# Optimization experiments

Measured on AMD Instinct MI355X. Metric: run time of the kernel, lower is better.

Reference implementation:

```python
import jax, jax.numpy as jnp
import numpy as np

# Static configuration (matches init_kwargs / input_specs)
B = 4          # number of point clouds (equal-sized)
NPER = 4096    # points per cloud
RATIO = 0.25
MPER = int(NPER * RATIO)  # sampled centroids per cloud
R = 0.2        # ball-query radius
K = 64         # max_num_neighbors
C = 64         # feature dim


def setup_inputs() -> dict:
    key = jax.random.key(0)
    ks = jax.random.split(key, 6)
    N = B * NPER
    x = jax.random.normal(ks[0], (N, C), dtype=jnp.float32)
    pos = jax.random.uniform(ks[1], (N, 3), dtype=jnp.float32)
    batch = (jnp.arange(N) // NPER).astype(jnp.int64)
    weight = jax.random.normal(ks[2], (N,), dtype=jnp.float32)
    # local_nn = Seq(Lin(67,128), ReLU, Lin(128,256), ReLU)
    W1 = jax.random.normal(ks[3], (C + 3, 128), dtype=jnp.float32) / np.float32(np.sqrt(C + 3))
    b1 = jnp.zeros((128,), dtype=jnp.float32)
    W2 = jax.random.normal(ks[4], (128, 256), dtype=jnp.float32) / np.float32(np.sqrt(128))
    b2 = jnp.zeros((256,), dtype=jnp.float32)
    return {"x": x, "pos": pos, "batch": batch, "weight": weight,
            "W1": W1, "b1": b1, "W2": W2, "b2": b2}


def _fps_single(p):
    """Farthest point sampling on one cloud p:[NPER,3] -> MPER int32 indices.
    Deterministic start at index 0 (torch_geometric uses a random start)."""
    n = p.shape[0]
    def step(carry, _):
        mind, last = carry
        d = jnp.sum((p - p[last]) ** 2, axis=-1)
        mind = jnp.minimum(mind, d)
        nxt = jnp.argmax(mind).astype(jnp.int32)
        return (mind, nxt), last
    init = (jnp.full((n,), jnp.inf, dtype=p.dtype), jnp.int32(0))
    _, idx = jax.lax.scan(step, init, None, length=MPER)
    return idx  # [MPER]


def reference(x, pos, batch, weight, W1, b1, W2, b2):
    pos_b = pos.reshape(B, NPER, 3)
    x_b = x.reshape(B, NPER, C)

    # --- FPS per cloud (vectorized over clouds) ---
    idx = jax.vmap(_fps_single)(pos_b)                      # [B, MPER] local indices

    qpos = jnp.take_along_axis(pos_b, idx[:, :, None], axis=1)  # [B, MPER, 3]

    # --- radius ball query: K nearest within r (fixed-size, batch-respecting) ---
    d2 = jnp.sum((qpos[:, :, None, :] - pos_b[:, None, :, :]) ** 2, axis=-1)  # [B,MPER,NPER]
    neg, nbr = jax.lax.top_k(-d2, K)                        # [B, MPER, K]
    valid = (-neg) <= jnp.float32(R * R)                    # [B, MPER, K]

    # --- gather neighbor features / positions ---
    flat = nbr.reshape(B, MPER * K)
    x_j = jnp.take_along_axis(x_b, flat[:, :, None], axis=1).reshape(B, MPER, K, C)
    pos_j = jnp.take_along_axis(pos_b, flat[:, :, None], axis=1).reshape(B, MPER, K, 3)
    rel = pos_j - qpos[:, :, None, :]                       # [B, MPER, K, 3]

    # --- PointNetConv: local_nn(concat(x_j, rel)) then max aggregation ---
    msg = jnp.concatenate([x_j, rel], axis=-1)              # [B, MPER, K, C+3]
    h = jax.nn.relu(jnp.einsum('bmkc,cd->bmkd', msg, W1) + b1)
    h = jax.nn.relu(jnp.einsum('bmkd,de->bmke', h, W2) + b2)
    h = jnp.where(valid[:, :, :, None], h, -jnp.inf)
    x_out = jnp.max(h, axis=2).reshape(B * MPER, -1)        # [B*MPER, 256]

    # --- gather sampled pos / batch / weight using global indices ---
    idx_g = (idx + (jnp.arange(B, dtype=jnp.int32) * NPER)[:, None]).reshape(-1)
    pos_out = pos[idx_g]
    batch_out = batch[idx_g]
    weight_out = weight[idx_g]
    return x_out, pos_out, batch_out, weight_out
```

## Files before the change

kernel.cpp:

```cpp
#include <hip/hip_runtime.h>

#define NPER 4096
#define MPER 1024
#define KNB 64
#define NB 4
#define CAP 1024

typedef __attribute__((ext_vector_type(8))) short short8_t;
typedef __attribute__((ext_vector_type(4))) float f32x4;
typedef __attribute__((ext_vector_type(2))) float f32x2;

__device__ __forceinline__ unsigned short f2bf(float f) {
  union { float f; unsigned u; } v; v.f = f;
  unsigned r = v.u + 0x7fffu + ((v.u >> 16) & 1u);
  return (unsigned short)(r >> 16);
}

__device__ __forceinline__ f32x2 pk_add(f32x2 a, f32x2 b) {
  f32x2 d; asm("v_pk_add_f32 %0, %1, %2" : "=v"(d) : "v"(a), "v"(b)); return d;
}
__device__ __forceinline__ f32x2 pk_mul(f32x2 a, f32x2 b) {
  f32x2 d; asm("v_pk_mul_f32 %0, %1, %2" : "=v"(d) : "v"(a), "v"(b)); return d;
}

__device__ __forceinline__ void lds_barrier() {
  asm volatile("s_waitcnt lgkmcnt(0)" ::: "memory");
  __builtin_amdgcn_s_barrier();
  asm volatile("" ::: "memory");
}

#define DPP_KEY_STEP(ctrl)                                                            \
  {                                                                                   \
    unsigned lo = (unsigned)k, hi = (unsigned)(k >> 32);                              \
    unsigned tlo = (unsigned)__builtin_amdgcn_update_dpp((int)lo, (int)lo, ctrl, 0xF, 0xF, false); \
    unsigned thi = (unsigned)__builtin_amdgcn_update_dpp((int)hi, (int)hi, ctrl, 0xF, 0xF, false); \
    unsigned long long tk = ((unsigned long long)thi << 32) | tlo;                    \
    if (tk > k) k = tk;                                                               \
  }

#define U64MAX(a, b) (((a) > (b)) ? (a) : (b))

__global__ __launch_bounds__(256) void prep_kernel(const float* __restrict__ W1,
                                                   const float* __restrict__ W2,
                                                   unsigned short* __restrict__ w1f,
                                                   unsigned short* __restrict__ w2f,
                                                   int* __restrict__ idxg,
                                                   int* __restrict__ control) {
  const int f = blockIdx.x * 256 + threadIdx.x;
  if (f < 12288) {
    const int frag = f >> 9, r = f & 511, lane = r >> 3, e = r & 7;
    const int nt = frag / 3, kt = frag % 3;
    const int n = nt * 16 + (lane & 15);
    const int k = kt * 32 + (lane >> 4) * 8 + e;
    float v = (k < 67) ? W1[k * 128 + n] : 0.f;
    w1f[f] = f2bf(v);
  } else if (f < 45056) {
    const int g = f - 12288;
    const int frag = g >> 9, r = g & 511, lane = r >> 3, e = r & 7;
    const int nt = frag >> 2, kt = frag & 3;
    const int n = nt * 16 + (lane & 15);
    const int k = kt * 32 + (lane >> 4) * 8 + e;
    w2f[g] = f2bf(W2[k * 256 + n]);
  } else if (f < 45056 + NB * MPER) {
    idxg[f - 45056] = -1;
  } else if (f < 45056 + NB * MPER + 8) {
    control[f - 45056 - NB * MPER] = 0;
  }
}

__global__ __launch_bounds__(256) void fused_kernel(const float* __restrict__ x,
                                                    const float* __restrict__ pos,
                                                    const float* __restrict__ weight,
                                                    const unsigned short* __restrict__ w1f,
                                                    const unsigned short* __restrict__ w2f,
                                                    const float* __restrict__ b1,
                                                    const float* __restrict__ b2,
                                                    int* __restrict__ idxg,
                                                    int* __restrict__ control,
                                                    float* __restrict__ out) {
  __shared__ float4 p4[NPER];
  __shared__ alignas(16) unsigned long long candk[2][4];
  __shared__ int s_idx[MPER];
  __shared__ float cd[CAP];
  __shared__ int   ci[CAP];
  __shared__ int   s_cnt;
  __shared__ alignas(16) unsigned short s_msg[64][104];
  __shared__ alignas(16) unsigned short s_h1[64][136];
  __shared__ int   s_valid[64];
  __shared__ float s_red[4][256];
  __shared__ int   s_w, s_qi;

  int* ctr = control;

  const int t = threadIdx.x;
  const int wave = t >> 6, lane = t & 63;

  if (blockIdx.x < NB) {
    const int b = blockIdx.x;
    const int base = b * NPER;
    const int wid = wave;

    for (int i = t; i < NPER; i += 256) {
      p4[i] = make_float4(pos[(size_t)(base + i) * 3 + 0],
                          pos[(size_t)(base + i) * 3 + 1],
                          pos[(size_t)(base + i) * 3 + 2], 0.f);
    }
    __syncthreads();

    f32x2 pxp[8], pyp[8], pzp[8];
    float mnd[16];
    const int i0 = t * 16;
#pragma unroll
    for (int p = 0; p < 8; ++p) {
      float4 a = p4[i0 + 2 * p];
      float4 c = p4[i0 + 2 * p + 1];
      pxp[p] = (f32x2){a.x, c.x};
      pyp[p] = (f32x2){a.y, c.y};
      pzp[p] = (f32x2){a.z, c.z};
    }
#pragma unroll
    for (int j = 0; j < 16; ++j) mnd[j] = __builtin_inff();

    int last = 0;
    for (int it = 0; it < MPER; ++it) {
      if (t == 0) s_idx[it] = last;
      if (wid == 0 && lane < 32 && (it & 31) == 0 && it != 0) {
        int v = s_idx[it - 32 + lane];
        __hip_atomic_store(&idxg[b * MPER + it - 32 + lane], v,
                           __ATOMIC_RELAXED, __HIP_MEMORY_SCOPE_AGENT);
      }
      if (it == MPER - 1) break;
      const float4 q = p4[last];
      const f32x2 nqx = (f32x2){-q.x, -q.x};
      const f32x2 nqy = (f32x2){-q.y, -q.y};
      const f32x2 nqz = (f32x2){-q.z, -q.z};
      float bv = -1.0f; int bj = 0;
#pragma unroll
      for (int p = 0; p < 8; ++p) {
        f32x2 dx = pk_add(pxp[p], nqx);
        f32x2 dy = pk_add(pyp[p], nqy);
        f32x2 dz = pk_add(pzp[p], nqz);
        f32x2 s = pk_add(pk_add(pk_mul(dx, dx), pk_mul(dy, dy)), pk_mul(dz, dz));
        float m0 = fminf(mnd[2 * p], s.x);     mnd[2 * p] = m0;
        if (m0 > bv) { bv = m0; bj = 2 * p; }
        float m1 = fminf(mnd[2 * p + 1], s.y); mnd[2 * p + 1] = m1;
        if (m1 > bv) { bv = m1; bj = 2 * p + 1; }
      }
      const int bi = i0 + bj;
      union { float f; unsigned u; } fu; fu.f = bv;
      unsigned long long k = ((unsigned long long)fu.u << 32) | (0xFFFFFFFFu - (unsigned)bi);
      DPP_KEY_STEP(0x128)
      DPP_KEY_STEP(0x124)
      DPP_KEY_STEP(0x122)
      DPP_KEY_STEP(0x121)
      DPP_KEY_STEP(0x142)
      DPP_KEY_STEP(0x143)
      if (lane == 63) candk[it & 1][wid] = k;
      lds_barrier();
      const ulonglong2* ck = (const ulonglong2*)&candk[it & 1][0];
      ulonglong2 c0 = ck[0], c1 = ck[1];
      unsigned long long m0 = U64MAX(c0.x, c0.y);
      unsigned long long m1 = U64MAX(c1.x, c1.y);
      unsigned long long mg = U64MAX(m0, m1);
      last = (int)(0xFFFFFFFFu - (unsigned)mg);
    }
    lds_barrier();
    if (wid == 0 && lane < 32) {
      int v = s_idx[992 + lane];
      __hip_atomic_store(&idxg[b * MPER + 992 + lane], v,
                         __ATOMIC_RELAXED, __HIP_MEMORY_SCOPE_AGENT);
    }
    return;
  }

  for (;;) {
    if (t == 0) {
      s_cnt = 0;
      s_w = atomicAdd(ctr, 1);
    }
    __syncthreads();
    const int w = s_w;
    if (w >= NB * MPER) return;
    const int cloud = w & 3;
    const int m = w >> 2;
    const int c = cloud * MPER + m;
    const int base = cloud * NPER;

    if (t == 0) {
      int v;
      while ((v = __hip_atomic_load(&idxg[c], __ATOMIC_RELAXED,
                                    __HIP_MEMORY_SCOPE_AGENT)) < 0)
        __builtin_amdgcn_s_sleep(8);
      s_qi = v;
    }
    __syncthreads();
    const int qi = s_qi;

    const float q0 = pos[(size_t)(base + qi) * 3 + 0];
    const float q1 = pos[(size_t)(base + qi) * 3 + 1];
    const float q2 = pos[(size_t)(base + qi) * 3 + 2];
    const float r2f = (float)(0.2 * 0.2);

#pragma unroll
    for (int s = 0; s < 16; ++s) {
      const int i = t + s * 256;
      float dx = __fsub_rn(q0, pos[(size_t)(base + i) * 3 + 0]);
      float dy = __fsub_rn(q1, pos[(size_t)(base + i) * 3 + 1]);
      float dz = __fsub_rn(q2, pos[(size_t)(base + i) * 3 + 2]);
      float d = __fadd_rn(__fadd_rn(__fmul_rn(dx, dx), __fmul_rn(dy, dy)), __fmul_rn(dz, dz));
      if (d <= r2f) {
        int p = atomicAdd(&s_cnt, 1);
        if (p < CAP) { cd[p] = d; ci[p] = i; }
      }
    }
    __syncthreads();
    int n = s_cnt; if (n > CAP) n = CAP;
    if (n > KNB) {
      int P = 64; while (P < n) P <<= 1;
      for (int i = n + t; i < P; i += 256) { cd[i] = __builtin_inff(); ci[i] = 0x7fffffff; }
      __syncthreads();
      for (int k2 = 2; k2 <= P; k2 <<= 1) {
        for (int j = k2 >> 1; j > 0; j >>= 1) {
          for (int i = t; i < P; i += 256) {
            const int ixj = i ^ j;
            if (ixj > i) {
              const bool up = ((i & k2) == 0);
              float a = cd[i], bb = cd[ixj];
              int ia = ci[i], ib = ci[ixj];
              const bool gt = (a > bb) || (a == bb && ia > ib);
              if (gt == up) { cd[i] = bb; cd[ixj] = a; ci[i] = ib; ci[ixj] = ia; }
            }
          }
          __syncthreads();
        }
      }
    }

    const int nn = (n < KNB) ? n : KNB;
    const int nbrv = (lane < nn) ? ci[lane] : -1;
    s_valid[lane] = (lane < nn) ? 1 : 0;

#pragma unroll 4
    for (int i = 0; i < 16; ++i) {
      const int k = wave * 16 + i;
      const int j = __shfl(nbrv, k, 64);
      float f = 0.f;
      if (j >= 0) f = x[(size_t)(base + j) * 64 + lane];
      s_msg[k][lane] = f2bf(f);
      if (lane < 40) {
        float rv = 0.f;
        if (lane < 3 && j >= 0) {
          float p = pos[(size_t)(base + j) * 3 + lane];
          float qq = (lane == 0) ? q0 : ((lane == 1) ? q1 : q2);
          rv = __fsub_rn(p, qq);
        }
        s_msg[k][64 + lane] = f2bf(rv);
      }
    }
    __syncthreads();

    const int row = wave * 16 + (lane & 15);
    const int kofs = (lane >> 4) * 8;

    short8_t a1[3];
#pragma unroll
    for (int kt = 0; kt < 3; ++kt)
      a1[kt] = *(const short8_t*)&s_msg[row][kt * 32 + kofs];
    f32x4 acc1[8];
#pragma unroll
    for (int nt = 0; nt < 8; ++nt) acc1[nt] = (f32x4){0.f, 0.f, 0.f, 0.f};
#pragma unroll
    for (int kt = 0; kt < 3; ++kt) {
#pragma unroll
      for (int nt = 0; nt < 8; ++nt) {
        short8_t bf = *(const short8_t*)&w1f[((nt * 3 + kt) * 64 + lane) * 8];
        acc1[nt] = __builtin_amdgcn_mfma_f32_16x16x32_bf16(a1[kt], bf, acc1[nt], 0, 0, 0);
      }
    }
#pragma unroll
    for (int nt = 0; nt < 8; ++nt) {
      const int n2 = nt * 16 + (lane & 15);
      const float bias = b1[n2];
      f32x4 v = acc1[nt];
#pragma unroll
      for (int e = 0; e < 4; ++e) {
        const int mm = wave * 16 + (lane >> 4) * 4 + e;
        float h = v[e] + bias;
        h = (h > 0.f) ? h : 0.f;
        s_h1[mm][n2] = f2bf(h);
      }
    }
    __syncthreads();

    short8_t a2[4];
#pragma unroll
    for (int kt = 0; kt < 4; ++kt)
      a2[kt] = *(const short8_t*)&s_h1[row][kt * 32 + kofs];
    f32x4 acc2[16];
#pragma unroll
    for (int nt = 0; nt < 16; ++nt) acc2[nt] = (f32x4){0.f, 0.f, 0.f, 0.f};
#pragma unroll
    for (int kt = 0; kt < 4; ++kt) {
#pragma unroll
      for (int nt = 0; nt < 16; ++nt) {
        short8_t bf = *(const short8_t*)&w2f[((nt * 4 + kt) * 64 + lane) * 8];
        acc2[nt] = __builtin_amdgcn_mfma_f32_16x16x32_bf16(a2[kt], bf, acc2[nt], 0, 0, 0);
      }
    }
    const int m0i = wave * 16 + (lane >> 4) * 4;
    const int vld0 = s_valid[m0i + 0], vld1 = s_valid[m0i + 1];
    const int vld2 = s_valid[m0i + 2], vld3 = s_valid[m0i + 3];
#pragma unroll
    for (int nt = 0; nt < 16; ++nt) {
      const int n2 = nt * 16 + (lane & 15);
      const float bias = b2[n2];
      f32x4 d = acc2[nt];
      float best = -__builtin_inff();
      {
        float h;
        h = d[0] + bias; h = (h > 0.f) ? h : 0.f; if (vld0) best = fmaxf(best, h);
        h = d[1] + bias; h = (h > 0.f) ? h : 0.f; if (vld1) best = fmaxf(best, h);
        h = d[2] + bias; h = (h > 0.f) ? h : 0.f; if (vld2) best = fmaxf(best, h);
        h = d[3] + bias; h = (h > 0.f) ? h : 0.f; if (vld3) best = fmaxf(best, h);
      }
      best = fmaxf(best, __shfl_xor(best, 16, 64));
      best = fmaxf(best, __shfl_xor(best, 32, 64));
      if ((lane >> 4) == 0) s_red[wave][n2] = best;
    }
    __syncthreads();
    const float r = fmaxf(fmaxf(s_red[0][t], s_red[1][t]), fmaxf(s_red[2][t], s_red[3][t]));
    out[(size_t)c * 256 + t] = r;

    if (t < 5) {
      const int g = base + qi;
      float* pos_out = out + 1048576;
      float* batch_out = out + 1048576 + 12288;
      float* w_out = out + 1048576 + 12288 + 4096;
      if (t < 3)      pos_out[c * 3 + t] = pos[(size_t)g * 3 + t];
      else if (t == 3) batch_out[c] = (float)cloud;
      else             w_out[c] = weight[g];
    }
    __syncthreads();
  }
}

extern "C" void kernel_launch(void* const* d_in, const int* in_sizes, int n_in,
                              void* d_out, int out_size, void* d_ws, size_t ws_size,
                              hipStream_t stream) {
  const float* x      = (const float*)d_in[0];
  const float* pos    = (const float*)d_in[1];
  const float* weight = (const float*)d_in[3];
  const float* W1     = (const float*)d_in[4];
  const float* b1     = (const float*)d_in[5];
  const float* W2     = (const float*)d_in[6];
  const float* b2     = (const float*)d_in[7];
  float* out = (float*)d_out;

  char* ws = (char*)d_ws;
  int* idxg = (int*)ws;
  unsigned short* w1f = (unsigned short*)(ws + 16384);
  unsigned short* w2f = (unsigned short*)(ws + 40960);
  int* control = (int*)(ws + 106496);

  prep_kernel<<<193, 256, 0, stream>>>(W1, W2, w1f, w2f, idxg, control);
  fused_kernel<<<256, 256, 0, stream>>>(x, pos, weight, w1f, w2f, b1, b2,
                                        idxg, control, out);
}
```

Measured before the change: 672.3 us.

## Run FPS on a single wave per cloud to drop the per-iteration block barrier

The farthest point sampling loop now runs on one 64-lane wave per cloud instead of four waves. Each lane holds 64 min-distances in registers and reads point coordinates from LDS on every iteration. The cross-wave LDS candidate exchange and barrier are replaced by a DPP reduction plus a readlane, and the chosen index is written to global memory every iteration instead of in batches of 32. This removes the serial barrier latency from each of the 1023 iterations, at the cost of four times the arithmetic per lane, extra LDS reads and higher register pressure.

```diff
diff --git a/kernel.cpp b/kernel.cpp
--- a/kernel.cpp
+++ b/kernel.cpp
@@ -21,12 +21,6 @@
 }
 __device__ __forceinline__ f32x2 pk_mul(f32x2 a, f32x2 b) {
   f32x2 d; asm("v_pk_mul_f32 %0, %1, %2" : "=v"(d) : "v"(a), "v"(b)); return d;
-}
-
-__device__ __forceinline__ void lds_barrier() {
-  asm volatile("s_waitcnt lgkmcnt(0)" ::: "memory");
-  __builtin_amdgcn_s_barrier();
-  asm volatile("" ::: "memory");
 }
 
 #define DPP_KEY_STEP(ctrl)                                                            \
@@ -37,8 +31,6 @@
     unsigned long long tk = ((unsigned long long)thi << 32) | tlo;                    \
     if (tk > k) k = tk;                                                               \
   }
-
-#define U64MAX(a, b) (((a) > (b)) ? (a) : (b))
 
 __global__ __launch_bounds__(256) void prep_kernel(const float* __restrict__ W1,
                                                    const float* __restrict__ W2,
@@ -79,8 +71,6 @@
                                                     int* __restrict__ control,
                                                     float* __restrict__ out) {
   __shared__ float4 p4[NPER];
-  __shared__ alignas(16) unsigned long long candk[2][4];
-  __shared__ int s_idx[MPER];
   __shared__ float cd[CAP];
   __shared__ int   ci[CAP];
   __shared__ int   s_cnt;
@@ -98,7 +88,6 @@
   if (blockIdx.x < NB) {
     const int b = blockIdx.x;
     const int base = b * NPER;
-    const int wid = wave;
 
     for (int i = t; i < NPER; i += 256) {
       p4[i] = make_float4(pos[(size_t)(base + i) * 3 + 0],
@@ -106,47 +95,41 @@
                           pos[(size_t)(base + i) * 3 + 2], 0.f);
     }
     __syncthreads();
-
-    f32x2 pxp[8], pyp[8], pzp[8];
-    float mnd[16];
-    const int i0 = t * 16;
-#pragma unroll
-    for (int p = 0; p < 8; ++p) {
-      float4 a = p4[i0 + 2 * p];
-      float4 c = p4[i0 + 2 * p + 1];
-      pxp[p] = (f32x2){a.x, c.x};
-      pyp[p] = (f32x2){a.y, c.y};
-      pzp[p] = (f32x2){a.z, c.z};
-    }
-#pragma unroll
-    for (int j = 0; j < 16; ++j) mnd[j] = __builtin_inff();
+    if (t >= 64) return;
+
+    float mnd[64];
+#pragma unroll
+    for (int j = 0; j < 64; ++j) mnd[j] = __builtin_inff();
+    const float4* pb = &p4[t];
 
     int last = 0;
     for (int it = 0; it < MPER; ++it) {
-      if (t == 0) s_idx[it] = last;
-      if (wid == 0 && lane < 32 && (it & 31) == 0 && it != 0) {
-        int v = s_idx[it - 32 + lane];
-        __hip_atomic_store(&idxg[b * MPER + it - 32 + lane], v,
+      if (t == 0)
+        __hip_atomic_store(&idxg[b * MPER + it], last,
                            __ATOMIC_RELAXED, __HIP_MEMORY_SCOPE_AGENT);
-      }
       if (it == MPER - 1) break;
       const float4 q = p4[last];
       const f32x2 nqx = (f32x2){-q.x, -q.x};
       const f32x2 nqy = (f32x2){-q.y, -q.y};
       const f32x2 nqz = (f32x2){-q.z, -q.z};
-      float bv = -1.0f; int bj = 0;
-#pragma unroll
-      for (int p = 0; p < 8; ++p) {
-        f32x2 dx = pk_add(pxp[p], nqx);
-        f32x2 dy = pk_add(pyp[p], nqy);
-        f32x2 dz = pk_add(pzp[p], nqz);
+      float bv = -1.0f; int bslot = 0;
+#pragma unroll
+      for (int j = 0; j < 32; ++j) {
+        const float4 a = pb[128 * j];
+        const float4 c = pb[128 * j + 64];
+        f32x2 px = (f32x2){a.x, c.x};
+        f32x2 py = (f32x2){a.y, c.y};
+        f32x2 pz = (f32x2){a.z, c.z};
+        f32x2 dx = pk_add(px, nqx);
+        f32x2 dy = pk_add(py, nqy);
+        f32x2 dz = pk_add(pz, nqz);
         f32x2 s = pk_add(pk_add(pk_mul(dx, dx), pk_mul(dy, dy)), pk_mul(dz, dz));
-        float m0 = fminf(mnd[2 * p], s.x);     mnd[2 * p] = m0;
-        if (m0 > bv) { bv = m0; bj = 2 * p; }
-        float m1 = fminf(mnd[2 * p + 1], s.y); mnd[2 * p + 1] = m1;
-        if (m1 > bv) { bv = m1; bj = 2 * p + 1; }
-      }
-      const int bi = i0 + bj;
+        float m0 = fminf(mnd[2 * j], s.x);     mnd[2 * j] = m0;
+        if (m0 > bv) { bv = m0; bslot = 2 * j; }
+        float m1 = fminf(mnd[2 * j + 1], s.y); mnd[2 * j + 1] = m1;
+        if (m1 > bv) { bv = m1; bslot = 2 * j + 1; }
+      }
+      const int bi = t + (bslot << 6);
       union { float f; unsigned u; } fu; fu.f = bv;
       unsigned long long k = ((unsigned long long)fu.u << 32) | (0xFFFFFFFFu - (unsigned)bi);
       DPP_KEY_STEP(0x128)
@@ -155,20 +138,8 @@
       DPP_KEY_STEP(0x121)
       DPP_KEY_STEP(0x142)
       DPP_KEY_STEP(0x143)
-      if (lane == 63) candk[it & 1][wid] = k;
-      lds_barrier();
-      const ulonglong2* ck = (const ulonglong2*)&candk[it & 1][0];
-      ulonglong2 c0 = ck[0], c1 = ck[1];
-      unsigned long long m0 = U64MAX(c0.x, c0.y);
-      unsigned long long m1 = U64MAX(c1.x, c1.y);
-      unsigned long long mg = U64MAX(m0, m1);
-      last = (int)(0xFFFFFFFFu - (unsigned)mg);
-    }
-    lds_barrier();
-    if (wid == 0 && lane < 32) {
-      int v = s_idx[992 + lane];
-      __hip_atomic_store(&idxg[b * MPER + 992 + lane], v,
-                         __ATOMIC_RELAXED, __HIP_MEMORY_SCOPE_AGENT);
+      const int lo63 = __builtin_amdgcn_readlane((int)(unsigned)k, 63);
+      last = (int)(0xFFFFFFFFu - (unsigned)lo63);
     }
     return;
   }
```

New measurement: 2.645 ms. +293.4%, slower.
